# Optimization experiments

Hardware: AMD Instinct MI355X
Metric: run time of the kernel (lower is better)

The kernel has to match this reference:

```python
import jax, jax.numpy as jnp
import numpy as np
import math

B, T, D, H = 2, 4096, 2048, 16
HD = D // H  # 128
OFFSET = -math.log(math.sqrt(D)) + 1e-6  # q_offset == k_offset in the original


def setup_inputs() -> dict:
    key = jax.random.key(0)
    ks = jax.random.split(key, 7)
    s = 1.0 / np.sqrt(D).astype(np.float32)  # keep exp() in a sane range
    return {
        "hidden_states": jax.random.normal(ks[0], (B, T, D), jnp.float32),
        "Wq": jax.random.normal(ks[1], (D, D), jnp.float32) * s,
        "Wk": jax.random.normal(ks[2], (D, D), jnp.float32) * s,
        "Wv": jax.random.normal(ks[3], (D, D), jnp.float32) * s,
        "Wo": jax.random.normal(ks[4], (D, D), jnp.float32) * s,
        "Fq": jax.random.normal(ks[5], (D, D), jnp.float32) * s,  # q feature map
        "Fk": jax.random.normal(ks[6], (D, D), jnp.float32) * s,  # k feature map
    }


def _split_heads(x):
    # [B, T, D] -> [B, H, T, HD]
    return x.reshape(B, T, H, HD).transpose(0, 2, 1, 3)


def reference(hidden_states, Wq, Wk, Wv, Wo, Fq, Fk):
    q = hidden_states @ Wq
    k = hidden_states @ Wk
    v = hidden_states @ Wv
    # Performer-style positive feature maps
    q_prime = jnp.exp(q @ Fq + OFFSET)
    k_prime = jnp.exp(k @ Fk + OFFSET)
    q_p = _split_heads(q_prime)   # [B,H,T,HD]
    k_p = _split_heads(k_prime)
    v_h = _split_heads(v)
    # causal_attention1: q_t^T (k_t v_t^T) == (q_t . k_t) * v_t, then cumsum over T.
    # Equivalent to the original [B,H,T,HD,HD] outer-product + cumsum, without
    # materializing the huge intermediate.
    dot = jnp.einsum("bhtd,bhtd->bht", q_p, k_p)           # [B,H,T]
    att_raw = jnp.cumsum(dot[..., None] * v_h, axis=2)      # [B,H,T,HD]
    attn = att_raw / k_p                                    # att_norm = k_prime
    # merge heads: [B,H,T,HD] -> [B,T,D]
    attn = attn.transpose(0, 2, 1, 3).reshape(B, T, D)
    return attn @ Wo
```

## Files before the change

### kernel.cpp

```cpp
#include <hip/hip_runtime.h>
#include <hip/hip_bf16.h>
#include <cmath>

constexpr int Bc = 2, Tc = 4096, Dc = 2048, Hc = 16, HDc = 128;
constexpr int Mrows = Bc * Tc;
constexpr int NCHUNK = 32, CHUNK = 128;

__device__ __forceinline__ unsigned short f2bf(float x) {
  union { float f; unsigned int u; } v; v.f = x;
  unsigned int r = v.u + 0x7FFFu + ((v.u >> 16) & 1u);
  return (unsigned short)(r >> 16);
}
__device__ __forceinline__ float bf2f(unsigned short u) {
  union { unsigned int i; float f; } v; v.i = ((unsigned int)u) << 16;
  return v.f;
}

typedef __attribute__((ext_vector_type(8))) short bf16x8;
typedef __attribute__((ext_vector_type(4))) float f32x4;

__device__ __forceinline__ void gload16(const unsigned short* g, unsigned short* l) {
  __builtin_amdgcn_global_load_lds(
      (const __attribute__((address_space(1))) void*)(const void*)g,
      (__attribute__((address_space(3))) void*)(void*)l,
      16, 0, 0);
}

__global__ void cvt_bf16(const float* __restrict__ in, unsigned short* __restrict__ outp) {
  size_t i = ((size_t)blockIdx.x * 256 + threadIdx.x) * 4;
  float4 f = *(const float4*)(in + i);
  ushort4 u;
  u.x = f2bf(f.x); u.y = f2bf(f.y); u.z = f2bf(f.z); u.w = f2bf(f.w);
  *(ushort4*)(outp + i) = u;
}

__global__ void transpose_cvt(const float* __restrict__ W, unsigned short* __restrict__ Wt) {
  __shared__ float tile[32][33];
  int n0 = blockIdx.x * 32, k0 = blockIdx.y * 32;
  int tx = threadIdx.x & 31, ty = threadIdx.x >> 5;
#pragma unroll
  for (int i = 0; i < 4; ++i)
    tile[ty + 8 * i][tx] = W[(size_t)(k0 + ty + 8 * i) * Dc + n0 + tx];
  __syncthreads();
#pragma unroll
  for (int i = 0; i < 4; ++i)
    Wt[(size_t)(n0 + ty + 8 * i) * Dc + k0 + tx] = f2bf(tile[tx][ty + 8 * i]);
}

template <int EPI, int WMw, int WNw, int MI, int NI>
__global__ __launch_bounds__(WMw * WNw * 64, 2) void gemmP(
    const unsigned short* __restrict__ A0, const unsigned short* __restrict__ B0,
    void* __restrict__ C0, void* __restrict__ C1, void* __restrict__ C2,
    const unsigned short* __restrict__ A1, const unsigned short* __restrict__ B1,
    void* __restrict__ C1a,
    int M, int N, int lda, int ldc, float eoff) {
  constexpr int K = 2048;
  constexpr int NT = K / 32;
  constexpr int THREADS = WMw * WNw * 64;
  constexpr int BM = WMw * MI * 16;
  constexpr int BN = WNw * NI * 16;
  constexpr int ASLAB = BM * 32;
  constexpr int BSLAB = BN * 32;
  constexpr int BUF = ASLAB + BSLAB;
  constexpr int SROWS = THREADS / 4;
  static_assert(2 * SROWS == BM && BM == BN, "staging geometry");
  extern __shared__ unsigned short lds[];

  const unsigned short* A = A0;
  const unsigned short* Bt = B0;
  void* Cz = C0;
  if (blockIdx.y) { A = A1; Bt = B1; Cz = C1a; }

  const int tid = threadIdx.x;
  const int lane = tid & 63;
  const int wave = tid >> 6;
  const int wm = wave / WNw;
  const int wn = wave % WNw;

  const int nbn = N / BN;
  const int nwg = (M / BM) * nbn;
  const int bidx = (int)blockIdx.x;
  const int wgid = (bidx & 7) * (nwg >> 3) + (bidx >> 3);
  const int bm = wgid / nbn;
  const int bn = wgid % nbn;

  const int srow = tid >> 2;
  const int scolL = (tid & 3) << 3;
  const int scolG = scolL ^ ((srow & 6) << 2);
  const unsigned short* gA = A + (size_t)(bm * BM + srow) * lda + scolG;
  const unsigned short* gB = Bt + (size_t)(bn * BN + srow) * K + scolG;
  const int sstage = srow * 32 + scolL;
  const size_t arstep = (size_t)SROWS * lda;
  const size_t brstep = (size_t)SROWS * K;

  const int fr = lane & 15;
  const int fko = ((lane >> 4) << 3) ^ ((lane & 6) << 2);
  const int aoff = (wm * MI * 16 + fr) * 32 + fko;
  const int boff = ASLAB + (wn * NI * 16 + fr) * 32 + fko;

  f32x4 acc[MI][NI] = {};
  bf16x8 afr[MI / 2];
  bf16x8 bfr[NI];

#pragma unroll
  for (int t = 0; t < 3; ++t) {
    const unsigned short* sA = gA + t * 32;
    const unsigned short* sB = gB + t * 32;
    unsigned short* dst = lds + t * BUF;
    gload16(sA,          dst + sstage);
    gload16(sA + arstep, dst + sstage + SROWS * 32);
    gload16(sB,          dst + ASLAB + sstage);
    gload16(sB + brstep, dst + ASLAB + sstage + SROWS * 32);
  }
  asm volatile("s_waitcnt vmcnt(8)" ::: "memory");
  __builtin_amdgcn_s_barrier();

  for (int v = 0; v < NT; ++v) {
    const int rb = (v & 3) * BUF;
    const int wb = ((v + 3) & 3) * BUF;
    const int tn = (v + 3) & (NT - 1);
    const unsigned short* srcA = gA + tn * 32;
    const unsigned short* srcB = gB + tn * 32;

    {
#pragma unroll
      for (int mi = 0; mi < MI / 2; ++mi)
        afr[mi] = *(const bf16x8*)(lds + rb + aoff + mi * 512);
#pragma unroll
      for (int ni = 0; ni < NI; ++ni)
        bfr[ni] = *(const bf16x8*)(lds + rb + boff + ni * 512);
      gload16(srcA,          lds + wb + sstage);
      gload16(srcA + arstep, lds + wb + sstage + SROWS * 32);
      __builtin_amdgcn_s_barrier();
      asm volatile("s_waitcnt lgkmcnt(0)" ::: "memory");
      __builtin_amdgcn_s_setprio(1);
#pragma unroll
      for (int mi = 0; mi < MI / 2; ++mi)
#pragma unroll
        for (int ni = 0; ni < NI; ++ni)
          acc[mi][ni] = __builtin_amdgcn_mfma_f32_16x16x32_bf16(afr[mi], bfr[ni], acc[mi][ni], 0, 0, 0);
      __builtin_amdgcn_s_setprio(0);
      __builtin_amdgcn_s_barrier();
    }
    {
#pragma unroll
      for (int mi = 0; mi < MI / 2; ++mi)
        afr[mi] = *(const bf16x8*)(lds + rb + aoff + (MI / 2 + mi) * 512);
      gload16(srcB,          lds + wb + ASLAB + sstage);
      gload16(srcB + brstep, lds + wb + ASLAB + sstage + SROWS * 32);
      asm volatile("s_waitcnt vmcnt(8)" ::: "memory");
      __builtin_amdgcn_s_barrier();
      asm volatile("s_waitcnt lgkmcnt(0)" ::: "memory");
      __builtin_amdgcn_s_setprio(1);
#pragma unroll
      for (int mi = 0; mi < MI / 2; ++mi)
#pragma unroll
        for (int ni = 0; ni < NI; ++ni)
          acc[MI / 2 + mi][ni] = __builtin_amdgcn_mfma_f32_16x16x32_bf16(afr[mi], bfr[ni], acc[MI / 2 + mi][ni], 0, 0, 0);
      __builtin_amdgcn_s_setprio(0);
      __builtin_amdgcn_s_barrier();
    }
  }

  const int fq = lane >> 4;
  const int crow = bm * BM + wm * (MI * 16);
  if constexpr (EPI == 3) {
    const int seg = bn >> 3;
    unsigned short* outp = (unsigned short*)(seg == 0 ? C0 : (seg == 1 ? C1 : C2));
    const int ccol = (bn & 7) * BN + wn * (NI * 16) + fr;
#pragma unroll
    for (int mi = 0; mi < MI; ++mi)
#pragma unroll
      for (int ni = 0; ni < NI; ++ni)
#pragma unroll
        for (int ii = 0; ii < 4; ++ii) {
          const int r = crow + mi * 16 + fq * 4 + ii;
          const int c = ccol + ni * 16;
          float vv = acc[mi][ni][ii];
          if (seg < 2) vv = __expf(vv + eoff);
          outp[(size_t)r * ldc + c] = f2bf(vv);
        }
  } else {
    const int ccol = bn * BN + wn * (NI * 16) + fr;
#pragma unroll
    for (int mi = 0; mi < MI; ++mi)
#pragma unroll
      for (int ni = 0; ni < NI; ++ni)
#pragma unroll
        for (int ii = 0; ii < 4; ++ii) {
          const int r = crow + mi * 16 + fq * 4 + ii;
          const int c = ccol + ni * 16;
          const size_t idx = (size_t)r * ldc + c;
          float vv = acc[mi][ni][ii];
          if (EPI == 0) ((float*)Cz)[idx] = vv;
          else          ((unsigned short*)Cz)[idx] = f2bf(vv);
        }
  }
}

__global__ void dot_kernel(const unsigned short* __restrict__ qp,
                           const unsigned short* __restrict__ kp,
                           float* __restrict__ dotb) {
  const int BHT = Bc * Hc * Tc;
  const int lane = threadIdx.x & 63;
  const int qw = lane >> 4;
  const int j = lane & 15;
  const int gw = (blockIdx.x * blockDim.x + threadIdx.x) >> 6;
  const int nw = (gridDim.x * blockDim.x) >> 6;

  for (int flat = gw * 4 + qw; flat < BHT; flat += nw * 4) {
    const int bh = flat >> 12;
    const int t = flat & (Tc - 1);
    const int b = bh >> 4, h = bh & 15;
    const size_t base = ((size_t)(b * Tc + t)) * Dc + h * HDc + j * 8;
    bf16x8 q = *(const bf16x8*)(qp + base);
    bf16x8 k = *(const bf16x8*)(kp + base);
    float p = 0.f;
#pragma unroll
    for (int i = 0; i < 8; ++i)
      p += bf2f((unsigned short)q[i]) * bf2f((unsigned short)k[i]);
#pragma unroll
    for (int m = 8; m; m >>= 1) p += __shfl_xor(p, m);
    if (j == 0) dotb[flat] = p;
  }
}

__global__ void scan_chunks(const float* __restrict__ dotb,
                            const unsigned short* __restrict__ v,
                            float* __restrict__ chks) {
  int bid = blockIdx.x;
  int c = bid % NCHUNK, bh = bid / NCHUNK;
  int b = bh / Hc, h = bh % Hc;
  int d = threadIdx.x;
  const float* dp = dotb + (size_t)bh * Tc + c * CHUNK;
  const unsigned short* vp = v + ((size_t)(b * Tc + c * CHUNK)) * Dc + h * HDc + d;
  float acc = 0.f;
  for (int t = 0; t < CHUNK; ++t)
    acc += dp[t] * bf2f(vp[(size_t)t * Dc]);
  chks[(size_t)bid * HDc + d] = acc;
}

__global__ void scan_offsets(float* __restrict__ chks) {
  int bh = blockIdx.x;
  int d = threadIdx.x;
  float run = 0.f;
  for (int c = 0; c < NCHUNK; ++c) {
    size_t idx = ((size_t)bh * NCHUNK + c) * HDc + d;
    float tmp = chks[idx];
    chks[idx] = run;
    run += tmp;
  }
}

__global__ void scan_final(const float* __restrict__ dotb,
                           const unsigned short* __restrict__ v,
                           const unsigned short* __restrict__ kp,
                           const float* __restrict__ chks,
                           unsigned short* __restrict__ attn) {
  int bid = blockIdx.x;
  int c = bid % NCHUNK, bh = bid / NCHUNK;
  int b = bh / Hc, h = bh % Hc;
  int d = threadIdx.x;
  const float* dp = dotb + (size_t)bh * Tc + c * CHUNK;
  size_t base = ((size_t)(b * Tc + c * CHUNK)) * Dc + h * HDc + d;
  float acc = chks[(size_t)bid * HDc + d];
  for (int t = 0; t < CHUNK; ++t) {
    size_t idx = base + (size_t)t * Dc;
    acc += dp[t] * bf2f(v[idx]);
    attn[idx] = f2bf(acc / bf2f(kp[idx]));
  }
}

extern "C" void kernel_launch(void* const* d_in, const int* in_sizes, int n_in,
                              void* d_out, int out_size, void* d_ws, size_t ws_size,
                              hipStream_t stream) {
  const float* hs = (const float*)d_in[0];
  const float* Wq = (const float*)d_in[1];
  const float* Wk = (const float*)d_in[2];
  const float* Wv = (const float*)d_in[3];
  const float* Wo = (const float*)d_in[4];
  const float* Fq = (const float*)d_in[5];
  const float* Fk = (const float*)d_in[6];
  float* out = (float*)d_out;

  const size_t MD = (size_t)Mrows * Dc;
  const size_t DD = (size_t)Dc * Dc;

  char* w = (char*)d_ws;
  size_t off = 0;
  auto take = [&](size_t bytes) -> void* {
    void* r = w + off;
    off += (bytes + 255) & ~(size_t)255;
    return r;
  };

  unsigned short* hs_bf = (unsigned short*)take(MD * 2);
  unsigned short* wq_bf = (unsigned short*)take(DD * 2);
  unsigned short* wtfq  = (unsigned short*)take(DD * 2);
  unsigned short* wk_bf = (unsigned short*)take(DD * 2);
  unsigned short* wtfk  = (unsigned short*)take(DD * 2);
  unsigned short* wcat  = (unsigned short*)take(3 * DD * 2);
  unsigned short* wto   = (unsigned short*)take(DD * 2);
  unsigned short* Kp    = (unsigned short*)take(MD * 2);
  unsigned short* Vbf   = (unsigned short*)take(MD * 2);
  float* dotb = (float*)take((size_t)Bc * Hc * Tc * 4);
  float* chks = (float*)take((size_t)Bc * Hc * NCHUNK * HDc * 4);

  unsigned short* Qp = wq_bf;
  unsigned short* attnbf = hs_bf;

  const float OFF = (float)(-0.5 * log(2048.0) + 1e-6);

  (void)hipFuncSetAttribute((const void*)gemmP<0, 2, 4, 8, 4>, hipFuncAttributeMaxDynamicSharedMemorySize, 131072);
  (void)hipFuncSetAttribute((const void*)gemmP<3, 2, 4, 8, 4>, hipFuncAttributeMaxDynamicSharedMemorySize, 131072);
  (void)hipFuncSetAttribute((const void*)gemmP<1, 2, 2, 4, 4>, hipFuncAttributeMaxDynamicSharedMemorySize, 65536);

  cvt_bf16<<<(int)(MD / 1024), 256, 0, stream>>>(hs, hs_bf);
  cvt_bf16<<<(int)(DD / 1024), 256, 0, stream>>>(Wq, wq_bf);
  cvt_bf16<<<(int)(DD / 1024), 256, 0, stream>>>(Wk, wk_bf);

  dim3 tg(Dc / 32, Dc / 32);
  transpose_cvt<<<tg, 256, 0, stream>>>(Fq, wtfq);
  transpose_cvt<<<tg, 256, 0, stream>>>(Fk, wtfk);
  transpose_cvt<<<tg, 256, 0, stream>>>(Wv, wcat + 2 * DD);
  transpose_cvt<<<tg, 256, 0, stream>>>(Wo, wto);

  gemmP<1, 2, 2, 4, 4><<<dim3(256, 2), 256, 65536, stream>>>(
      wtfq, wq_bf, wcat, nullptr, nullptr,
      wtfk, wk_bf, wcat + DD,
      2048, 2048, 2048, 2048, 0.f);

  const int fblocks = (Mrows / 256) * (6144 / 256);
  gemmP<3, 2, 4, 8, 4><<<fblocks, 512, 131072, stream>>>(
      hs_bf, wcat, Qp, Kp, Vbf, nullptr, nullptr, nullptr,
      Mrows, 6144, Dc, Dc, OFF);

  dot_kernel<<<1024, 256, 0, stream>>>(Qp, Kp, dotb);

  scan_chunks<<<Bc * Hc * NCHUNK, 128, 0, stream>>>(dotb, Vbf, chks);
  scan_offsets<<<Bc * Hc, 128, 0, stream>>>(chks);
  scan_final<<<Bc * Hc * NCHUNK, 128, 0, stream>>>(dotb, Vbf, Kp, chks, attnbf);

  const int gblocks = (Mrows / 256) * (Dc / 256);
  gemmP<0, 2, 4, 8, 4><<<gblocks, 512, 131072, stream>>>(
      attnbf, wto, out, nullptr, nullptr, nullptr, nullptr, nullptr,
      Mrows, Dc, Dc, Dc, 0.f);
}
```

Measured before the change: 443.9 us.

## Load GEMM B fragments directly into registers and fuse small prep kernels

The GEMM kernel stops staging the B operand through LDS. Each lane now loads its B fragments straight from global memory into double-buffered registers, and only A goes through a 4-slot LDS ring. That halves LDS use, which may improve occupancy and drops the LDS round trip for B, but B reads are no longer coalesced or shared across waves. The weight conversion and transpose launches are batched into single kernels, and the dot product is fused with the chunk scan to cut launches and a re-read of the dot buffer.

New measurement: 614.9 us. 38.5% more time.

```diff
diff --git a/kernel.cpp b/kernel.cpp
--- a/kernel.cpp
+++ b/kernel.cpp
@@ -34,7 +34,28 @@
   *(ushort4*)(outp + i) = u;
 }
 
-__global__ void transpose_cvt(const float* __restrict__ W, unsigned short* __restrict__ Wt) {
+__global__ void cvt_bf16_2(const float* __restrict__ in0, unsigned short* __restrict__ out0,
+                           const float* __restrict__ in1, unsigned short* __restrict__ out1) {
+  const float* in = blockIdx.y ? in1 : in0;
+  unsigned short* op = blockIdx.y ? out1 : out0;
+  size_t i = ((size_t)blockIdx.x * 256 + threadIdx.x) * 4;
+  float4 f = *(const float4*)(in + i);
+  ushort4 u;
+  u.x = f2bf(f.x); u.y = f2bf(f.y); u.z = f2bf(f.z); u.w = f2bf(f.w);
+  *(ushort4*)(op + i) = u;
+}
+
+__global__ void transpose_cvt4(const float* __restrict__ W0, unsigned short* __restrict__ T0,
+                               const float* __restrict__ W1, unsigned short* __restrict__ T1,
+                               const float* __restrict__ W2, unsigned short* __restrict__ T2,
+                               const float* __restrict__ W3, unsigned short* __restrict__ T3) {
+  const float* W; unsigned short* Wt;
+  switch (blockIdx.z) {
+    case 0: W = W0; Wt = T0; break;
+    case 1: W = W1; Wt = T1; break;
+    case 2: W = W2; Wt = T2; break;
+    default: W = W3; Wt = T3; break;
+  }
   __shared__ float tile[32][33];
   int n0 = blockIdx.x * 32, k0 = blockIdx.y * 32;
   int tx = threadIdx.x & 31, ty = threadIdx.x >> 5;
@@ -48,7 +69,7 @@
 }
 
 template <int EPI, int WMw, int WNw, int MI, int NI>
-__global__ __launch_bounds__(WMw * WNw * 64, 2) void gemmP(
+__global__ __launch_bounds__(WMw * WNw * 64, 2) void gemmR(
     const unsigned short* __restrict__ A0, const unsigned short* __restrict__ B0,
     void* __restrict__ C0, void* __restrict__ C1, void* __restrict__ C2,
     const unsigned short* __restrict__ A1, const unsigned short* __restrict__ B1,
@@ -60,10 +81,9 @@
   constexpr int BM = WMw * MI * 16;
   constexpr int BN = WNw * NI * 16;
   constexpr int ASLAB = BM * 32;
-  constexpr int BSLAB = BN * 32;
-  constexpr int BUF = ASLAB + BSLAB;
   constexpr int SROWS = THREADS / 4;
-  static_assert(2 * SROWS == BM && BM == BN, "staging geometry");
+  static_assert(2 * SROWS == BM, "staging geometry");
+  static_assert(NI == 4, "vmcnt ledger assumes 4 B-loads/tile");
   extern __shared__ unsigned short lds[];
 
   const unsigned short* A = A0;
@@ -88,79 +108,84 @@
   const int scolL = (tid & 3) << 3;
   const int scolG = scolL ^ ((srow & 6) << 2);
   const unsigned short* gA = A + (size_t)(bm * BM + srow) * lda + scolG;
-  const unsigned short* gB = Bt + (size_t)(bn * BN + srow) * K + scolG;
   const int sstage = srow * 32 + scolL;
   const size_t arstep = (size_t)SROWS * lda;
-  const size_t brstep = (size_t)SROWS * K;
 
   const int fr = lane & 15;
   const int fko = ((lane >> 4) << 3) ^ ((lane & 6) << 2);
   const int aoff = (wm * MI * 16 + fr) * 32 + fko;
-  const int boff = ASLAB + (wn * NI * 16 + fr) * 32 + fko;
+
+  const unsigned short* gBr = Bt + (size_t)(bn * BN + wn * NI * 16 + fr) * K
+                                 + ((lane >> 4) << 3);
 
   f32x4 acc[MI][NI] = {};
-  bf16x8 afr[MI / 2];
-  bf16x8 bfr[NI];
-
-#pragma unroll
-  for (int t = 0; t < 3; ++t) {
-    const unsigned short* sA = gA + t * 32;
-    const unsigned short* sB = gB + t * 32;
-    unsigned short* dst = lds + t * BUF;
-    gload16(sA,          dst + sstage);
-    gload16(sA + arstep, dst + sstage + SROWS * 32);
-    gload16(sB,          dst + ASLAB + sstage);
-    gload16(sB + brstep, dst + ASLAB + sstage + SROWS * 32);
-  }
-  asm volatile("s_waitcnt vmcnt(8)" ::: "memory");
+  bf16x8 af[MI / 2];
+  bf16x8 bA[NI], bB[NI];
+
+  {
+    gload16(gA,          lds + sstage);
+    gload16(gA + arstep, lds + sstage + SROWS * 32);
+    gload16(gA + 32,          lds + ASLAB + sstage);
+    gload16(gA + 32 + arstep, lds + ASLAB + sstage + SROWS * 32);
+#pragma unroll
+    for (int ni = 0; ni < NI; ++ni)
+      bA[ni] = *(const bf16x8*)(gBr + (size_t)ni * 16 * K);
+  }
+  asm volatile("s_waitcnt vmcnt(6)" ::: "memory");
   __builtin_amdgcn_s_barrier();
 
-  for (int v = 0; v < NT; ++v) {
-    const int rb = (v & 3) * BUF;
-    const int wb = ((v + 3) & 3) * BUF;
-    const int tn = (v + 3) & (NT - 1);
-    const unsigned short* srcA = gA + tn * 32;
-    const unsigned short* srcB = gB + tn * 32;
-
-    {
-#pragma unroll
-      for (int mi = 0; mi < MI / 2; ++mi)
-        afr[mi] = *(const bf16x8*)(lds + rb + aoff + mi * 512);
-#pragma unroll
-      for (int ni = 0; ni < NI; ++ni)
-        bfr[ni] = *(const bf16x8*)(lds + rb + boff + ni * 512);
-      gload16(srcA,          lds + wb + sstage);
-      gload16(srcA + arstep, lds + wb + sstage + SROWS * 32);
-      __builtin_amdgcn_s_barrier();
-      asm volatile("s_waitcnt lgkmcnt(0)" ::: "memory");
-      __builtin_amdgcn_s_setprio(1);
-#pragma unroll
-      for (int mi = 0; mi < MI / 2; ++mi)
-#pragma unroll
-        for (int ni = 0; ni < NI; ++ni)
-          acc[mi][ni] = __builtin_amdgcn_mfma_f32_16x16x32_bf16(afr[mi], bfr[ni], acc[mi][ni], 0, 0, 0);
-      __builtin_amdgcn_s_setprio(0);
-      __builtin_amdgcn_s_barrier();
-    }
-    {
-#pragma unroll
-      for (int mi = 0; mi < MI / 2; ++mi)
-        afr[mi] = *(const bf16x8*)(lds + rb + aoff + (MI / 2 + mi) * 512);
-      gload16(srcB,          lds + wb + ASLAB + sstage);
-      gload16(srcB + brstep, lds + wb + ASLAB + sstage + SROWS * 32);
-      asm volatile("s_waitcnt vmcnt(8)" ::: "memory");
-      __builtin_amdgcn_s_barrier();
-      asm volatile("s_waitcnt lgkmcnt(0)" ::: "memory");
-      __builtin_amdgcn_s_setprio(1);
-#pragma unroll
-      for (int mi = 0; mi < MI / 2; ++mi)
-#pragma unroll
-        for (int ni = 0; ni < NI; ++ni)
-          acc[MI / 2 + mi][ni] = __builtin_amdgcn_mfma_f32_16x16x32_bf16(afr[mi], bfr[ni], acc[MI / 2 + mi][ni], 0, 0, 0);
-      __builtin_amdgcn_s_setprio(0);
-      __builtin_amdgcn_s_barrier();
-    }
-  }
+#define TILE_BODY(V, BC, BN_)                                                   \
+  {                                                                             \
+    const int rslot = ((V) & 3) * ASLAB;                                        \
+    const int wslot = (((V) + 2) & 3) * ASLAB;                                  \
+    const int tb = ((V) + 1) & (NT - 1);                                        \
+    const int ta = ((V) + 2) & (NT - 1);                                        \
+                \
+    _Pragma("unroll")                                                           \
+    for (int mi = 0; mi < MI / 2; ++mi)                                         \
+      af[mi] = *(const bf16x8*)(lds + rslot + aoff + mi * 512);                 \
+    _Pragma("unroll")                                                           \
+    for (int ni = 0; ni < NI; ++ni)                                             \
+      BN_[ni] = *(const bf16x8*)(gBr + (size_t)ni * 16 * K + tb * 32);          \
+    {                                                                           \
+      const unsigned short* sA = gA + ta * 32;                                  \
+      gload16(sA,          lds + wslot + sstage);                               \
+      gload16(sA + arstep, lds + wslot + sstage + SROWS * 32);                  \
+    }                                                                           \
+    __builtin_amdgcn_s_barrier();                                               \
+    asm volatile("s_waitcnt lgkmcnt(0)" ::: "memory");                          \
+    __builtin_amdgcn_s_setprio(1);                                              \
+    _Pragma("unroll")                                                           \
+    for (int mi = 0; mi < MI / 2; ++mi)                                         \
+      _Pragma("unroll")                                                         \
+      for (int ni = 0; ni < NI; ++ni)                                           \
+        acc[mi][ni] = __builtin_amdgcn_mfma_f32_16x16x32_bf16(                  \
+            af[mi], BC[ni], acc[mi][ni], 0, 0, 0);                              \
+    __builtin_amdgcn_s_setprio(0);                                              \
+    __builtin_amdgcn_s_barrier();                                               \
+                                                           \
+    _Pragma("unroll")                                                           \
+    for (int mi = 0; mi < MI / 2; ++mi)                                         \
+      af[mi] = *(const bf16x8*)(lds + rslot + aoff + (MI / 2 + mi) * 512);      \
+    __builtin_amdgcn_s_barrier();                                               \
+    asm volatile("s_waitcnt lgkmcnt(0)" ::: "memory");                          \
+    __builtin_amdgcn_s_setprio(1);                                              \
+    _Pragma("unroll")                                                           \
+    for (int mi = 0; mi < MI / 2; ++mi)                                         \
+      _Pragma("unroll")                                                         \
+      for (int ni = 0; ni < NI; ++ni)                                           \
+        acc[MI / 2 + mi][ni] = __builtin_amdgcn_mfma_f32_16x16x32_bf16(         \
+            af[mi], BC[ni], acc[MI / 2 + mi][ni], 0, 0, 0);                     \
+    __builtin_amdgcn_s_setprio(0);                                              \
+    asm volatile("s_waitcnt vmcnt(6)" ::: "memory");         \
+    __builtin_amdgcn_s_barrier();                                               \
+  }
+
+  for (int v = 0; v < NT; v += 2) {
+    TILE_BODY(v, bA, bB)
+    TILE_BODY(v + 1, bB, bA)
+  }
+#undef TILE_BODY
 
   const int fq = lane >> 4;
   const int crow = bm * BM + wm * (MI * 16);
@@ -198,20 +223,25 @@
   }
 }
 
-__global__ void dot_kernel(const unsigned short* __restrict__ qp,
+__global__ void dot_chunks(const unsigned short* __restrict__ qp,
                            const unsigned short* __restrict__ kp,
-                           float* __restrict__ dotb) {
-  const int BHT = Bc * Hc * Tc;
-  const int lane = threadIdx.x & 63;
-  const int qw = lane >> 4;
-  const int j = lane & 15;
-  const int gw = (blockIdx.x * blockDim.x + threadIdx.x) >> 6;
-  const int nw = (gridDim.x * blockDim.x) >> 6;
-
-  for (int flat = gw * 4 + qw; flat < BHT; flat += nw * 4) {
-    const int bh = flat >> 12;
-    const int t = flat & (Tc - 1);
-    const int b = bh >> 4, h = bh & 15;
+                           const unsigned short* __restrict__ v,
+                           float* __restrict__ dotb,
+                           float* __restrict__ chks) {
+  __shared__ float dt[CHUNK];
+  const int bid = blockIdx.x;
+  const int c = bid & (NCHUNK - 1);
+  const int bh = bid >> 5;
+  const int b = bh >> 4, h = bh & 15;
+  const int tid = threadIdx.x;
+  const int lane = tid & 63, wv = tid >> 6;
+  const int qw = lane >> 4, j = lane & 15;
+  const int t0 = c * CHUNK;
+
+#pragma unroll
+  for (int pass = 0; pass < 8; ++pass) {
+    const int tl = pass * 16 + wv * 4 + qw;
+    const int t = t0 + tl;
     const size_t base = ((size_t)(b * Tc + t)) * Dc + h * HDc + j * 8;
     bf16x8 q = *(const bf16x8*)(qp + base);
     bf16x8 k = *(const bf16x8*)(kp + base);
@@ -221,23 +251,20 @@
       p += bf2f((unsigned short)q[i]) * bf2f((unsigned short)k[i]);
 #pragma unroll
     for (int m = 8; m; m >>= 1) p += __shfl_xor(p, m);
-    if (j == 0) dotb[flat] = p;
-  }
-}
-
-__global__ void scan_chunks(const float* __restrict__ dotb,
-                            const unsigned short* __restrict__ v,
-                            float* __restrict__ chks) {
-  int bid = blockIdx.x;
-  int c = bid % NCHUNK, bh = bid / NCHUNK;
-  int b = bh / Hc, h = bh % Hc;
-  int d = threadIdx.x;
-  const float* dp = dotb + (size_t)bh * Tc + c * CHUNK;
-  const unsigned short* vp = v + ((size_t)(b * Tc + c * CHUNK)) * Dc + h * HDc + d;
-  float acc = 0.f;
-  for (int t = 0; t < CHUNK; ++t)
-    acc += dp[t] * bf2f(vp[(size_t)t * Dc]);
-  chks[(size_t)bid * HDc + d] = acc;
+    if (j == 0) {
+      dt[tl] = p;
+      dotb[(size_t)bh * Tc + t] = p;
+    }
+  }
+  __syncthreads();
+  if (tid < HDc) {
+    const int d = tid;
+    const unsigned short* vp = v + ((size_t)(b * Tc + t0)) * Dc + h * HDc + d;
+    float acc = 0.f;
+    for (int t = 0; t < CHUNK; ++t)
+      acc += dt[t] * bf2f(vp[(size_t)t * Dc]);
+    chks[(size_t)bid * HDc + d] = acc;
+  }
 }
 
 __global__ void scan_offsets(float* __restrict__ chks) {
@@ -311,38 +338,33 @@
 
   const float OFF = (float)(-0.5 * log(2048.0) + 1e-6);
 
-  (void)hipFuncSetAttribute((const void*)gemmP<0, 2, 4, 8, 4>, hipFuncAttributeMaxDynamicSharedMemorySize, 131072);
-  (void)hipFuncSetAttribute((const void*)gemmP<3, 2, 4, 8, 4>, hipFuncAttributeMaxDynamicSharedMemorySize, 131072);
-  (void)hipFuncSetAttribute((const void*)gemmP<1, 2, 2, 4, 4>, hipFuncAttributeMaxDynamicSharedMemorySize, 65536);
+  (void)hipFuncSetAttribute((const void*)gemmR<0, 2, 4, 8, 4>, hipFuncAttributeMaxDynamicSharedMemorySize, 65536);
+  (void)hipFuncSetAttribute((const void*)gemmR<3, 2, 4, 8, 4>, hipFuncAttributeMaxDynamicSharedMemorySize, 65536);
+  (void)hipFuncSetAttribute((const void*)gemmR<1, 2, 2, 4, 4>, hipFuncAttributeMaxDynamicSharedMemorySize, 32768);
 
   cvt_bf16<<<(int)(MD / 1024), 256, 0, stream>>>(hs, hs_bf);
-  cvt_bf16<<<(int)(DD / 1024), 256, 0, stream>>>(Wq, wq_bf);
-  cvt_bf16<<<(int)(DD / 1024), 256, 0, stream>>>(Wk, wk_bf);
-
-  dim3 tg(Dc / 32, Dc / 32);
-  transpose_cvt<<<tg, 256, 0, stream>>>(Fq, wtfq);
-  transpose_cvt<<<tg, 256, 0, stream>>>(Fk, wtfk);
-  transpose_cvt<<<tg, 256, 0, stream>>>(Wv, wcat + 2 * DD);
-  transpose_cvt<<<tg, 256, 0, stream>>>(Wo, wto);
-
-  gemmP<1, 2, 2, 4, 4><<<dim3(256, 2), 256, 65536, stream>>>(
+  cvt_bf16_2<<<dim3((int)(DD / 1024), 2), 256, 0, stream>>>(Wq, wq_bf, Wk, wk_bf);
+
+  transpose_cvt4<<<dim3(Dc / 32, Dc / 32, 4), 256, 0, stream>>>(
+      Fq, wtfq, Fk, wtfk, Wv, wcat + 2 * DD, Wo, wto);
+
+  gemmR<1, 2, 2, 4, 4><<<dim3(256, 2), 256, 32768, stream>>>(
       wtfq, wq_bf, wcat, nullptr, nullptr,
       wtfk, wk_bf, wcat + DD,
       2048, 2048, 2048, 2048, 0.f);
 
   const int fblocks = (Mrows / 256) * (6144 / 256);
-  gemmP<3, 2, 4, 8, 4><<<fblocks, 512, 131072, stream>>>(
+  gemmR<3, 2, 4, 8, 4><<<fblocks, 512, 65536, stream>>>(
       hs_bf, wcat, Qp, Kp, Vbf, nullptr, nullptr, nullptr,
       Mrows, 6144, Dc, Dc, OFF);
 
-  dot_kernel<<<1024, 256, 0, stream>>>(Qp, Kp, dotb);
-
-  scan_chunks<<<Bc * Hc * NCHUNK, 128, 0, stream>>>(dotb, Vbf, chks);
+  dot_chunks<<<Bc * Hc * NCHUNK, 256, 0, stream>>>(Qp, Kp, Vbf, dotb, chks);
+
   scan_offsets<<<Bc * Hc, 128, 0, stream>>>(chks);
   scan_final<<<Bc * Hc * NCHUNK, 128, 0, stream>>>(dotb, Vbf, Kp, chks, attnbf);
 
   const int gblocks = (Mrows / 256) * (Dc / 256);
-  gemmP<0, 2, 4, 8, 4><<<gblocks, 512, 131072, stream>>>(
+  gemmR<0, 2, 4, 8, 4><<<gblocks, 512, 65536, stream>>>(
       attnbf, wto, out, nullptr, nullptr, nullptr, nullptr, nullptr,
       Mrows, Dc, Dc, Dc, 0.f);
 }
```
